# Kernel optimization log

Hardware: AMD Instinct MI355X
Metric: run time of the kernel (lower is better)

The kernel has to match this reference:

```python
import jax, jax.numpy as jnp
import numpy as np

B, N, HW, PS, FHW = 16, 4096, 224, 8, 56

def _gelu(x):
    return jax.nn.gelu(x, approximate=True)  # tanh approximation, matches nn.GELU(approximate='tanh')

def _conv(x, w, b, stride):
    y = jax.lax.conv_general_dilated(x, w, (stride, stride), [(1, 1), (1, 1)],
                                     dimension_numbers=('NCHW', 'OIHW', 'NCHW'))
    return y + b[None, :, None, None]

def _embed(points):
    # for i in 0..11: append sin(2^i * p) then cos(2^i * p) -> [B,N,48]
    factors = 2.0 ** jnp.arange(12, dtype=points.dtype)
    scaled = points[..., None, :] * factors[:, None]          # [B,N,12,2]
    feats = jnp.concatenate([jnp.sin(scaled), jnp.cos(scaled)], axis=-1)  # [B,N,12,4]
    return feats.reshape(points.shape[0], points.shape[1], 48)

def _extract_patches(fmap, points):
    # fmap [B,C,H,W]; points in [0,1]; bilinear grid_sample, zeros padding, align_corners=True
    Bq, C, H, W = fmap.shape
    centers = points * 2.0 - 1.0
    step = 2.0 / (W - 1)
    half = (PS - 1) / 2.0
    offs = jnp.linspace(-half, half, PS, dtype=fmap.dtype) * step
    offx2d, offy2d = jnp.meshgrid(offs, offs, indexing='ij')   # [ps,ps]
    gx = centers[..., 0][..., None, None] + offx2d             # [B,N,ps,ps]
    gy = centers[..., 1][..., None, None] + offy2d
    # align_corners=True pixel coords
    ix = (gx + 1.0) * 0.5 * (W - 1)
    iy = (gy + 1.0) * 0.5 * (H - 1)
    x0f = jnp.floor(ix); y0f = jnp.floor(iy)
    x0 = x0f.astype(jnp.int32); y0 = y0f.astype(jnp.int32)
    x1 = x0 + 1; y1 = y0 + 1
    wx1 = ix - x0f; wx0 = 1.0 - wx1
    wy1 = iy - y0f; wy0 = 1.0 - wy1
    fflat = fmap.reshape(Bq, C, H * W)

    def corner(xi, yi, w):
        valid = ((xi >= 0) & (xi < W) & (yi >= 0) & (yi < H)).astype(fmap.dtype)
        idx = jnp.clip(yi, 0, H - 1) * W + jnp.clip(xi, 0, W - 1)   # [B,N,ps,ps]
        vals = jax.vmap(lambda f, i: f[:, i])(fflat, idx)           # [B,C,N,ps,ps]
        return vals * (w * valid)[:, None]

    out = (corner(x0, y0, wx0 * wy0) + corner(x1, y0, wx1 * wy0)
           + corner(x0, y1, wx0 * wy1) + corner(x1, y1, wx1 * wy1))  # [B,C,N,ps,ps]
    return out.transpose(0, 2, 1, 3, 4)                              # [B,N,C,ps,ps]

def setup_inputs():
    key = jax.random.key(0)
    ks = jax.random.split(key, 26)
    def w(k, shape):
        fan_in = int(np.prod(shape[1:]))
        return jax.random.normal(k, shape, jnp.float32) * (1.0 / np.sqrt(fan_in))
    inp = {
        'points': jax.random.uniform(ks[0], (B, N, 2), jnp.float32),
        'images': jax.random.normal(ks[1], (B, 3, HW, HW), jnp.float32),
        # plane encoder
        'pw1': w(ks[2], (16, 3, 3, 3)),  'pb1': jnp.zeros((16,), jnp.float32),
        'pw2': w(ks[3], (32, 16, 3, 3)), 'pb2': jnp.zeros((32,), jnp.float32),
        'pw3': w(ks[4], (4, 32, 3, 3)),  'pb3': jnp.zeros((4,), jnp.float32),
        # global encoder
        'gw1': w(ks[5], (4, 3, 3, 3)),   'gb1': jnp.zeros((4,), jnp.float32),
        'gw2': w(ks[6], (8, 4, 3, 3)),   'gb2': jnp.zeros((8,), jnp.float32),
        'gw3': w(ks[7], (16, 8, 3, 3)),  'gb3': jnp.zeros((16,), jnp.float32),
        'gw4': w(ks[8], (32, 16, 3, 3)), 'gb4': jnp.zeros((32,), jnp.float32),
        'gw5': w(ks[9], (64, 32, 3, 3)), 'gb5': jnp.zeros((64,), jnp.float32),
        # point encoder (torch Linear: [out,in])
        'lw1': w(ks[10], (256, 48)),  'lb1': jnp.zeros((256,), jnp.float32),
        'lw2': w(ks[11], (256, 256)), 'lb2': jnp.zeros((256,), jnp.float32),
        # head
        'hw1': w(ks[12], (512, 576)), 'hb1': jnp.zeros((512,), jnp.float32),
        'hw2': w(ks[13], (1, 512)),   'hb2': jnp.zeros((1,), jnp.float32),
    }
    return inp

def reference(points, images, pw1, pb1, pw2, pb2, pw3, pb3,
              gw1, gb1, gw2, gb2, gw3, gb3, gw4, gb4, gw5, gb5,
              lw1, lb1, lw2, lb2, hw1, hb1, hw2, hb2):
    # point branch
    pe = _embed(points)                                         # [B,N,48]
    pf = _gelu(pe @ lw1.T + lb1) @ lw2.T + lb2                  # [B,N,256]
    # plane encoder -> 4x56x56 fmap
    f = _gelu(_conv(images, pw1, pb1, 2))
    f = _gelu(_conv(f, pw2, pb2, 2))
    fmap = _gelu(_conv(f, pw3, pb3, 1))                         # [B,4,56,56]
    # global encoder -> [B,64]
    g = images
    for wg, bg in ((gw1, gb1), (gw2, gb2), (gw3, gb3), (gw4, gb4), (gw5, gb5)):
        g = _gelu(_conv(g, wg, bg, 2))
    gc = g.mean(axis=(2, 3))                                    # AvgPool2d(7)+Flatten -> [B,64]
    gc = jnp.broadcast_to(gc[:, None, :], (points.shape[0], points.shape[1], 64))
    # per-point bilinear patch gather
    patches = _extract_patches(fmap, points).reshape(points.shape[0], points.shape[1], -1)  # [B,N,256]
    fused = jnp.concatenate([pf, patches, gc], axis=-1)         # [B,N,576]
    logit = _gelu(fused @ hw1.T + hb1) @ hw2.T + hb2            # [B,N,1]
    return logit
```

## Files before the change

kernel.cpp:

```cpp
#include <hip/hip_runtime.h>
#include <math.h>

#define BB 16
#define NN 4096
#define M_TOT (BB*NN)
#define TBK 32

typedef __attribute__((ext_vector_type(8))) short s8v;
typedef __attribute__((ext_vector_type(4))) float f4v;

__device__ __forceinline__ float gelu_t(float x){
    float u = 1.5957691216057308f * x * (1.0f + 0.044715f*x*x);
    return x / (1.0f + __expf(-u));
}

__device__ __forceinline__ unsigned short f2bf(float f){
    unsigned int u = __float_as_uint(f);
    u += 0x7fffu + ((u >> 16) & 1u);
    return (unsigned short)(u >> 16);
}

#define GLL(src, dst) __builtin_amdgcn_global_load_lds( \
    (const __attribute__((address_space(1))) void*)(src), \
    (__attribute__((address_space(3))) void*)(dst), 16, 0, 0)

template<int CIN, int COUT, int STRIDE, int CHUNK>
__device__ __forceinline__ void conv_dev2(
    const float* __restrict__ in, const float* __restrict__ w,
    const float* __restrict__ bias, float* __restrict__ out,
    int Hin, int Win, int Hout, int Wout, int bx, int by, int b, float* tile)
{
    constexpr int IW = 15*STRIDE + 3;
    constexpr int IH = IW;
    constexpr int PITCH = IW + 1;
    int tid = threadIdx.x;
    int tx = tid & 15, ty = tid >> 4;
    int wo = bx*16 + tx;
    int ho = by*16 + ty;
    int win0 = bx*16*STRIDE - 1;
    int hin0 = by*16*STRIDE - 1;
    bool valid = (wo < Wout) && (ho < Hout);

    float acc[COUT];
    #pragma unroll
    for (int co = 0; co < COUT; ++co) acc[co] = bias[co];

    const float* ib = in + (size_t)(b*CIN)*Hin*Win;
    for (int ci0 = 0; ci0 < CIN; ci0 += CHUNK) {
        __syncthreads();
        for (int idx = tid; idx < CHUNK*IH*IW; idx += 256) {
            int c = idx / (IH*IW), rem = idx - c*(IH*IW);
            int r = rem / IW, cc = rem - r*IW;
            int hi = hin0 + r, wi = win0 + cc;
            float v = 0.f;
            if ((unsigned)hi < (unsigned)Hin && (unsigned)wi < (unsigned)Win)
                v = ib[(size_t)(ci0 + c)*Hin*Win + hi*Win + wi];
            tile[c*IH*PITCH + r*PITCH + cc] = v;
        }
        __syncthreads();
        for (int ci = 0; ci < CHUNK; ++ci) {
            float vv[9];
            const float* tb = tile + ci*IH*PITCH;
            #pragma unroll
            for (int kh = 0; kh < 3; ++kh)
                #pragma unroll
                for (int kw = 0; kw < 3; ++kw)
                    vv[kh*3+kw] = tb[(ty*STRIDE + kh)*PITCH + tx*STRIDE + kw];
            const float* wc = w + (ci0 + ci)*9;
            #pragma unroll
            for (int co = 0; co < COUT; ++co) {
                const float* wp = wc + co*CIN*9;
                #pragma unroll
                for (int k = 0; k < 9; ++k)
                    acc[co] = fmaf(vv[k], wp[k], acc[co]);
            }
        }
    }
    if (valid) {
        size_t obase = ((size_t)b*COUT)*Hout*Wout + (size_t)ho*Wout + wo;
        #pragma unroll
        for (int co = 0; co < COUT; ++co)
            out[obase + (size_t)co*Hout*Wout] = gelu_t(acc[co]);
    }
}

__global__ __launch_bounds__(256) void conv_dual_k(
    const float* __restrict__ in,
    const float* __restrict__ wA, const float* __restrict__ bA,
    const float* __restrict__ wB, const float* __restrict__ bB,
    float* __restrict__ outA, float* __restrict__ outB)
{
    __shared__ float tile[3*33*34];
    const int Hin = 224, Win = 224, Hout = 112, Wout = 112;
    int tid = threadIdx.x;
    int tx = tid & 15, ty = tid >> 4;
    int b = blockIdx.z;
    int wo = blockIdx.x*16 + tx;
    int ho = blockIdx.y*16 + ty;
    int win0 = blockIdx.x*32 - 1;
    int hin0 = blockIdx.y*32 - 1;

    const float* ib = in + (size_t)(b*3)*Hin*Win;
    for (int idx = tid; idx < 3*1089; idx += 256) {
        int c = idx / 1089, rem = idx - c*1089;
        int r = rem / 33, cc = rem - r*33;
        int hi = hin0 + r, wi = win0 + cc;
        float v = 0.f;
        if ((unsigned)hi < (unsigned)Hin && (unsigned)wi < (unsigned)Win)
            v = ib[(size_t)c*Hin*Win + hi*Win + wi];
        tile[c*33*34 + r*34 + cc] = v;
    }
    __syncthreads();

    float accA[16], accB[4];
    #pragma unroll
    for (int co = 0; co < 16; ++co) accA[co] = bA[co];
    #pragma unroll
    for (int co = 0; co < 4; ++co) accB[co] = bB[co];

    #pragma unroll
    for (int ci = 0; ci < 3; ++ci) {
        float vv[9];
        const float* tb = tile + ci*33*34;
        #pragma unroll
        for (int kh = 0; kh < 3; ++kh)
            #pragma unroll
            for (int kw = 0; kw < 3; ++kw)
                vv[kh*3+kw] = tb[(ty*2 + kh)*34 + tx*2 + kw];
        #pragma unroll
        for (int co = 0; co < 16; ++co) {
            const float* wp = wA + co*27 + ci*9;
            #pragma unroll
            for (int k = 0; k < 9; ++k) accA[co] = fmaf(vv[k], wp[k], accA[co]);
        }
        #pragma unroll
        for (int co = 0; co < 4; ++co) {
            const float* wp = wB + co*27 + ci*9;
            #pragma unroll
            for (int k = 0; k < 9; ++k) accB[co] = fmaf(vv[k], wp[k], accB[co]);
        }
    }
    size_t px = (size_t)ho*Wout + wo;
    #pragma unroll
    for (int co = 0; co < 16; ++co)
        outA[((size_t)(b*16 + co))*Hout*Wout + px] = gelu_t(accA[co]);
    #pragma unroll
    for (int co = 0; co < 4; ++co)
        outB[((size_t)(b*4 + co))*Hout*Wout + px] = gelu_t(accB[co]);
}

__global__ __launch_bounds__(256) void conv_pg2_k(
    const float* __restrict__ f1, const float* __restrict__ pw2, const float* __restrict__ pb2, float* __restrict__ f2,
    const float* __restrict__ g1, const float* __restrict__ gw2, const float* __restrict__ gb2, float* __restrict__ g2)
{
    __shared__ float tile[8*33*34];
    int z = blockIdx.z;
    if (z < 32) {
        int b = z >> 1, half = z & 1;
        conv_dev2<16,16,2,8>(f1 + (size_t)b*16*12544, pw2 + half*2304, pb2 + half*16,
                             f2 + ((size_t)(b*32 + half*16))*3136,
                             112,112, 56,56, blockIdx.x, blockIdx.y, 0, tile);
    } else {
        conv_dev2<4,8,2,4>(g1, gw2, gb2, g2, 112,112, 56,56, blockIdx.x, blockIdx.y, z-32, tile);
    }
}

__global__ __launch_bounds__(256) void conv_pg3_k(
    const float* __restrict__ f2, const float* __restrict__ pw3, const float* __restrict__ pb3, float4* __restrict__ fmap4,
    const float* __restrict__ g2, const float* __restrict__ gw3, const float* __restrict__ gb3, float* __restrict__ g3)
{
    __shared__ float tile[8*33*34];
    int z = blockIdx.z;
    if (z < 16) {
        int b = z;
        int idx = blockIdx.x*256 + threadIdx.x;
        if (idx >= 3136) return;
        int ho = idx / 56, wo = idx - ho*56;
        const float* ib = f2 + (size_t)b*32*3136;
        float acc[4];
        #pragma unroll
        for (int co = 0; co < 4; ++co) acc[co] = pb3[co];
        for (int ci = 0; ci < 32; ++ci) {
            const float* ic = ib + (size_t)ci*3136;
            #pragma unroll
            for (int kh = 0; kh < 3; ++kh) {
                int hi = ho - 1 + kh;
                if ((unsigned)hi >= 56u) continue;
                #pragma unroll
                for (int kw = 0; kw < 3; ++kw) {
                    int wi = wo - 1 + kw;
                    if ((unsigned)wi >= 56u) continue;
                    float v = ic[hi*56 + wi];
                    int wofs = ci*9 + kh*3 + kw;
                    #pragma unroll
                    for (int co = 0; co < 4; ++co)
                        acc[co] = fmaf(v, pw3[co*288 + wofs], acc[co]);
                }
            }
        }
        float4 o;
        o.x = gelu_t(acc[0]); o.y = gelu_t(acc[1]);
        o.z = gelu_t(acc[2]); o.w = gelu_t(acc[3]);
        fmap4[(size_t)b*3136 + idx] = o;
    } else {
        if (blockIdx.x >= 4) return;
        int bx = blockIdx.x & 1, by = blockIdx.x >> 1;
        conv_dev2<8,16,2,8>(g2, gw3, gb3, g3, 56,56, 28,28, bx, by, z-16, tile);
    }
}

__global__ __launch_bounds__(256) void g4_k(
    const float* __restrict__ g3, const float* __restrict__ w4,
    const float* __restrict__ b4, float* __restrict__ g4o)
{
    int idx = blockIdx.x*256 + threadIdx.x;
    int co = idx & 31;
    int t = idx >> 5;
    int b = t / 196, px = t - b*196;
    int ho = px / 14, wo = px - ho*14;
    const float* src = g3 + (size_t)b*16*784;
    const float* wp = w4 + co*144;
    float acc = b4[co];
    for (int ci = 0; ci < 16; ++ci) {
        #pragma unroll
        for (int kh = 0; kh < 3; ++kh) {
            int hi = ho*2 - 1 + kh;
            if ((unsigned)hi >= 28u) continue;
            #pragma unroll
            for (int kw = 0; kw < 3; ++kw) {
                int wi = wo*2 - 1 + kw;
                if ((unsigned)wi >= 28u) continue;
                acc = fmaf(src[ci*784 + hi*28 + wi], wp[ci*9 + kh*3 + kw], acc);
            }
        }
    }
    g4o[(size_t)b*6272 + px*32 + co] = gelu_t(acc);
}

__global__ __launch_bounds__(256) void g5_k(
    const float* __restrict__ g4o, const float* __restrict__ w5,
    const float* __restrict__ b5, float* __restrict__ gc)
{
    int idx = blockIdx.x*256 + threadIdx.x;
    int co = idx & 63;
    int t = idx >> 6;
    int b = t / 49, px = t - b*49;
    int ho = px / 7, wo = px - ho*7;
    const float* src = g4o + (size_t)b*6272;
    const float* wp = w5 + co*288;
    float acc = b5[co];
    for (int ci = 0; ci < 32; ++ci) {
        #pragma unroll
        for (int kh = 0; kh < 3; ++kh) {
            int hi = ho*2 - 1 + kh;
            if ((unsigned)hi >= 14u) continue;
            #pragma unroll
            for (int kw = 0; kw < 3; ++kw) {
                int wi = wo*2 - 1 + kw;
                if ((unsigned)wi >= 14u) continue;
                acc = fmaf(src[(hi*14 + wi)*32 + ci], wp[ci*9 + kh*3 + kw], acc);
            }
        }
    }
    atomicAdd(&gc[b*64 + co], gelu_t(acc) * (1.0f/49.0f));
}

__global__ void cvtall_k(const float* __restrict__ lw1, const float* __restrict__ lw2,
                         const float* __restrict__ hw1, unsigned short* __restrict__ blw1,
                         unsigned short* __restrict__ blw2, unsigned short* __restrict__ bhw1,
                         float* __restrict__ out, const float* __restrict__ b2,
                         float* __restrict__ gc){
    int i = blockIdx.x*blockDim.x + threadIdx.x;
    if (i < M_TOT) out[i] = b2[0];
    if (i < 1024) gc[i] = 0.f;
    if (i < 256*64) {
        int r = i >> 6, c = i & 63;
        blw1[i] = (c < 48) ? f2bf(lw1[r*48 + c]) : 0;
        return;
    }
    int j = i - 256*64;
    if (j < 256*256) { blw2[j] = f2bf(lw2[j]); return; }
    j -= 256*256;
    if (j < 512*576) bhw1[j] = f2bf(hw1[j]);
}

__global__ __launch_bounds__(512) void mlp12_k(
    const float* __restrict__ points,
    const unsigned short* __restrict__ W1, const float* __restrict__ b1,
    const unsigned short* __restrict__ W2, const float* __restrict__ b2,
    unsigned short* __restrict__ C,
    const float4* __restrict__ fmap4, const float* __restrict__ gc)
{
    __shared__ unsigned short Hd[128*256];
    __shared__ unsigned short B2[256*TBK];
    int tid = threadIdx.x;
    int wv = tid >> 6, lane = tid & 63;
    int q = lane >> 4, lr = lane & 15;
    int mi = wv >> 2, ni = wv & 3;
    size_t m0 = (size_t)blockIdx.x * 128;

    f4v acc1[4][4];
    #pragma unroll
    for (int i = 0; i < 4; ++i)
        #pragma unroll
        for (int j = 0; j < 4; ++j) acc1[i][j] = (f4v){0.f,0.f,0.f,0.f};

    #pragma unroll
    for (int kb = 0; kb < 2; ++kb) {
        int seg = kb*4 + q;
        s8v a[4], b[4];
        #pragma unroll
        for (int t = 0; t < 4; ++t) {
            size_t m = m0 + mi*64 + t*16 + lr;
            float px = points[m*2], py = points[m*2+1];
            union { s8v v; unsigned short u[8]; } pk;
            #pragma unroll
            for (int j = 0; j < 8; ++j) {
                int k = seg*8 + j;
                unsigned short val = 0;
                if (k < 48) {
                    int i2 = k >> 2, rr = k & 3;
                    float f = (float)(1 << i2);
                    float p = (rr & 1) ? py : px;
                    float s = f * p;
                    val = f2bf((rr < 2) ? __sinf(s) : __cosf(s));
                }
                pk.u[j] = val;
            }
            a[t] = pk.v;
        }
        #pragma unroll
        for (int t = 0; t < 4; ++t) {
            int n = ni*64 + t*16 + lr;
            b[t] = *(const s8v*)(W1 + n*64 + seg*8);
        }
        #pragma unroll
        for (int mt = 0; mt < 4; ++mt)
            #pragma unroll
            for (int nt = 0; nt < 4; ++nt)
                acc1[mt][nt] = __builtin_amdgcn_mfma_f32_16x16x32_bf16(a[mt], b[nt], acc1[mt][nt], 0, 0, 0);
    }
    {
        float b1v[4];
        #pragma unroll
        for (int nt = 0; nt < 4; ++nt) b1v[nt] = b1[ni*64 + nt*16 + lr];
        #pragma unroll
        for (int mt = 0; mt < 4; ++mt)
            #pragma unroll
            for (int r4 = 0; r4 < 4; ++r4) {
                int row = mi*64 + mt*16 + q*4 + r4;
                #pragma unroll
                for (int nt = 0; nt < 4; ++nt) {
                    int col = ni*64 + nt*16 + lr;
                    float v = gelu_t(acc1[mt][nt][r4] + b1v[nt]);
                    int p = (col >> 3) ^ (row & 7);
                    Hd[(row*32 + p)*8 + (col & 7)] = f2bf(v);
                }
            }
    }
    __syncthreads();

    f4v acc2[4][4];
    #pragma unroll
    for (int i = 0; i < 4; ++i)
        #pragma unroll
        for (int j = 0; j < 4; ++j) acc2[i][j] = (f4v){0.f,0.f,0.f,0.f};

    for (int kt = 0; kt < 8; ++kt) {
        #pragma unroll
        for (int r = 0; r < 2; ++r) {
            int f = r*512 + tid;
            int rr = f >> 2, ll = (f & 3) ^ ((f >> 3) & 3);
            GLL(W2 + rr*256 + kt*32 + ll*8, B2 + f*8);
        }
        __syncthreads();
        s8v a[4], b[4];
        int sw = q ^ ((lr >> 1) & 3);
        #pragma unroll
        for (int t = 0; t < 4; ++t) {
            int row = mi*64 + t*16 + lr;
            int p = (kt*4 + q) ^ (row & 7);
            a[t] = *(const s8v*)(Hd + (row*32 + p)*8);
        }
        #pragma unroll
        for (int t = 0; t < 4; ++t) {
            int n = ni*64 + t*16 + lr;
            b[t] = *(const s8v*)(B2 + (n*4 + sw)*8);
        }
        #pragma unroll
        for (int mt = 0; mt < 4; ++mt)
            #pragma unroll
            for (int nt = 0; nt < 4; ++nt)
                acc2[mt][nt] = __builtin_amdgcn_mfma_f32_16x16x32_bf16(a[mt], b[nt], acc2[mt][nt], 0, 0, 0);
        __syncthreads();
    }
    {
        float b2v[4];
        #pragma unroll
        for (int nt = 0; nt < 4; ++nt) b2v[nt] = b2[ni*64 + nt*16 + lr];
        #pragma unroll
        for (int mt = 0; mt < 4; ++mt)
            #pragma unroll
            for (int r4 = 0; r4 < 4; ++r4) {
                size_t m = m0 + mi*64 + mt*16 + q*4 + r4;
                #pragma unroll
                for (int nt = 0; nt < 4; ++nt) {
                    int n = ni*64 + nt*16 + lr;
                    C[m*576 + n] = f2bf(acc2[mt][nt][r4] + b2v[nt]);
                }
            }
    }
    #pragma unroll 1
    for (int it = 0; it < 16; ++it) {
        int task = it*512 + tid;
        int ml = task >> 6, ij = task & 63;
        size_t m = m0 + ml;
        int i = ij >> 3, j = ij & 7;
        int b = (int)(m >> 12);
        float px = points[m*2], py = points[m*2+1];
        float cx = px*2.f - 1.f, cy = py*2.f - 1.f;
        const float step = 2.0f/55.0f;
        float gx = cx + ((float)i - 3.5f)*step;
        float gy = cy + ((float)j - 3.5f)*step;
        float ix = (gx + 1.f)*0.5f*55.f;
        float iy = (gy + 1.f)*0.5f*55.f;
        float x0f = floorf(ix), y0f = floorf(iy);
        int x0 = (int)x0f, y0 = (int)y0f;
        int x1 = x0 + 1,  y1 = y0 + 1;
        float wx1 = ix - x0f, wx0 = 1.f - wx1;
        float wy1 = iy - y0f, wy0 = 1.f - wy1;
        float v00 = ((x0>=0)&&(x0<56)&&(y0>=0)&&(y0<56)) ? 1.f : 0.f;
        float v10 = ((x1>=0)&&(x1<56)&&(y0>=0)&&(y0<56)) ? 1.f : 0.f;
        float v01 = ((x0>=0)&&(x0<56)&&(y1>=0)&&(y1<56)) ? 1.f : 0.f;
        float v11 = ((x1>=0)&&(x1<56)&&(y1>=0)&&(y1<56)) ? 1.f : 0.f;
        float w00 = wx0*wy0*v00, w10 = wx1*wy0*v10, w01 = wx0*wy1*v01, w11 = wx1*wy1*v11;
        int cx0 = min(max(x0,0),55), cx1 = min(max(x1,0),55);
        int cy0 = min(max(y0,0),55), cy1 = min(max(y1,0),55);
        const float4* fb = fmap4 + (size_t)b*3136;
        float4 f00 = fb[cy0*56 + cx0], f10 = fb[cy0*56 + cx1];
        float4 f01 = fb[cy1*56 + cx0], f11 = fb[cy1*56 + cx1];
        float4 v;
        v.x = w00*f00.x + w10*f10.x + w01*f01.x + w11*f11.x;
        v.y = w00*f00.y + w10*f10.y + w01*f01.y + w11*f11.y;
        v.z = w00*f00.z + w10*f10.z + w01*f01.z + w11*f11.z;
        v.w = w00*f00.w + w10*f10.w + w01*f01.w + w11*f11.w;
        C[m*576 + 256 +   0 + ij] = f2bf(v.x);
        C[m*576 + 256 +  64 + ij] = f2bf(v.y);
        C[m*576 + 256 + 128 + ij] = f2bf(v.z);
        C[m*576 + 256 + 192 + ij] = f2bf(v.w);
        C[m*576 + 512 + ij] = f2bf(gc[b*64 + ij]);
    }
}

__global__ __launch_bounds__(256, 3) void gemm_hd_k(
    const unsigned short* __restrict__ A,
    const unsigned short* __restrict__ W,
    const float* __restrict__ bias, const float* __restrict__ w2,
    float* __restrict__ out)
{
    __shared__ unsigned short As[64*TBK];
    __shared__ unsigned short Bs[256*TBK];
    __shared__ float red[4*64];
    int tid = threadIdx.x;
    int wv = tid >> 6, lane = tid & 63;
    int q = lane >> 4, lr = lane & 15;
    int sw = q ^ ((lr >> 1) & 3);
    int nq = wv * 64;
    size_t m0 = (size_t)blockIdx.x * 64;
    int nbase = blockIdx.y * 256;

    int rA = tid >> 2;
    int lA = (tid & 3) ^ ((tid >> 3) & 3);
    const unsigned short* srcA = A + (m0 + rA)*576 + lA*8;
    unsigned short* dstA = As + tid*8;
    const unsigned short* srcB[4]; unsigned short* dstB[4];
    #pragma unroll
    for (int r = 0; r < 4; ++r) {
        int f = r*256 + tid;
        int rr = f >> 2, ll = (f & 3) ^ ((f >> 3) & 3);
        srcB[r] = W + (size_t)(nbase + rr)*576 + ll*8;
        dstB[r] = Bs + f*8;
    }

    f4v acc[4][4];
    #pragma unroll
    for (int i = 0; i < 4; ++i)
        #pragma unroll
        for (int j = 0; j < 4; ++j) acc[i][j] = (f4v){0.f,0.f,0.f,0.f};

    for (int k0 = 0; k0 < 576; k0 += TBK) {
        GLL(srcA, dstA); srcA += TBK;
        #pragma unroll
        for (int r = 0; r < 4; ++r) { GLL(srcB[r], dstB[r]); srcB[r] += TBK; }
        __syncthreads();
        s8v a[4], b[4];
        #pragma unroll
        for (int t = 0; t < 4; ++t)
            a[t] = *(const s8v*)(As + (t*16 + lr)*TBK + sw*8);
        #pragma unroll
        for (int t = 0; t < 4; ++t)
            b[t] = *(const s8v*)(Bs + (nq + t*16 + lr)*TBK + sw*8);
        #pragma unroll
        for (int mt = 0; mt < 4; ++mt)
            #pragma unroll
            for (int nt = 0; nt < 4; ++nt)
                acc[mt][nt] = __builtin_amdgcn_mfma_f32_16x16x32_bf16(a[mt], b[nt], acc[mt][nt], 0, 0, 0);
        __syncthreads();
    }
    float bv[4], w2v[4];
    #pragma unroll
    for (int nt = 0; nt < 4; ++nt) {
        int n = nbase + nq + nt*16 + lr;
        bv[nt] = bias[n];
        w2v[nt] = w2[n];
    }
    #pragma unroll
    for (int mt = 0; mt < 4; ++mt)
        #pragma unroll
        for (int r4 = 0; r4 < 4; ++r4) {
            int ml = mt*16 + q*4 + r4;
            float s = 0.f;
            #pragma unroll
            for (int nt = 0; nt < 4; ++nt)
                s += gelu_t(acc[mt][nt][r4] + bv[nt]) * w2v[nt];
            #pragma unroll
            for (int off = 8; off > 0; off >>= 1) s += __shfl_down(s, off, 16);
            if (lr == 0) red[wv*64 + ml] = s;
        }
    __syncthreads();
    if (tid < 64) {
        float t = red[tid] + red[64 + tid] + red[128 + tid] + red[192 + tid];
        atomicAdd(&out[m0 + tid], t);
    }
}

extern "C" void kernel_launch(void* const* d_in, const int* in_sizes, int n_in,
                              void* d_out, int out_size, void* d_ws, size_t ws_size,
                              hipStream_t stream) {
    const float* points = (const float*)d_in[0];
    const float* images = (const float*)d_in[1];
    const float* pw1 = (const float*)d_in[2];  const float* pb1 = (const float*)d_in[3];
    const float* pw2 = (const float*)d_in[4];  const float* pb2 = (const float*)d_in[5];
    const float* pw3 = (const float*)d_in[6];  const float* pb3 = (const float*)d_in[7];
    const float* gw1 = (const float*)d_in[8];  const float* gb1 = (const float*)d_in[9];
    const float* gw2 = (const float*)d_in[10]; const float* gb2 = (const float*)d_in[11];
    const float* gw3 = (const float*)d_in[12]; const float* gb3 = (const float*)d_in[13];
    const float* gw4 = (const float*)d_in[14]; const float* gb4 = (const float*)d_in[15];
    const float* gw5 = (const float*)d_in[16]; const float* gb5 = (const float*)d_in[17];
    const float* lw1 = (const float*)d_in[18]; const float* lb1 = (const float*)d_in[19];
    const float* lw2 = (const float*)d_in[20]; const float* lb2 = (const float*)d_in[21];
    const float* hw1 = (const float*)d_in[22]; const float* hb1 = (const float*)d_in[23];
    const float* hw2 = (const float*)d_in[24]; const float* hb2 = (const float*)d_in[25];
    float* out = (float*)d_out;

    char* base = (char*)d_ws;
    unsigned short* fused_b = (unsigned short*)base;
    unsigned short* hid_b   = fused_b + (size_t)M_TOT*576;
    float4* fmap4 = (float4*)(hid_b + (size_t)M_TOT*256);
    float* gc   = (float*)(fmap4 + (size_t)16*3136);
    unsigned short* blw1 = (unsigned short*)(gc + 1024);
    unsigned short* blw2 = blw1 + 256*64;
    unsigned short* bhw1 = blw2 + 256*256;
    float* ct = (float*)base;
    float* f1 = ct;
    float* f2 = f1 + (size_t)16*16*112*112;
    float* g1 = f2 + (size_t)16*32*56*56;
    float* g2 = g1 + (size_t)16*4*112*112;
    float* g3 = g2 + (size_t)16*8*56*56;
    float* g4 = g3 + (size_t)16*16*28*28;

    cvtall_k<<<1472, 256, 0, stream>>>(lw1, lw2, hw1, blw1, blw2, bhw1, out, hb2, gc);
    conv_dual_k<<<dim3(7,7,16), 256, 0, stream>>>(images, pw1, pb1, gw1, gb1, f1, g1);
    conv_pg2_k<<<dim3(4,4,48), 256, 0, stream>>>(f1, pw2, pb2, f2, g1, gw2, gb2, g2);
    conv_pg3_k<<<dim3(13,1,32), 256, 0, stream>>>(f2, pw3, pb3, fmap4, g2, gw3, gb3, g3);
    g4_k<<<392, 256, 0, stream>>>(g3, gw4, gb4, g4);
    g5_k<<<196, 256, 0, stream>>>(g4, gw5, gb5, gc);
    mlp12_k<<<M_TOT/128, 512, 0, stream>>>(points, blw1, lb1, blw2, lb2, fused_b, fmap4, gc);
    gemm_hd_k<<<dim3(M_TOT/64, 2), 256, 0, stream>>>(fused_b, bhw1, hb1, hw2, out);
}
```

Baseline: 433.3 us.

## Fuse point MLP, patch gather and head GEMM into one kernel via LDS

Merges mlp12_k and gemm_hd_k into a single mega kernel. Each 64-row tile now keeps its 576-wide fused feature row in swizzled LDS instead of writing it to a global bf16 buffer and reading it back. Each block covers all 512 head outputs, so the final sum is written directly with the bias instead of atomically added, and the output init is dropped from cvtall_k. The cost is a large LDS footprint (about 105 KB) that limits occupancy, more accumulators per wave (4x8 tiles), and W2 B-fragments read straight from global memory without LDS staging.

Result: slower. 486.1 us (+12.2%).

```diff
diff --git a/kernel.cpp b/kernel.cpp
--- a/kernel.cpp
+++ b/kernel.cpp
@@ -23,6 +23,12 @@
 #define GLL(src, dst) __builtin_amdgcn_global_load_lds( \
     (const __attribute__((address_space(1))) void*)(src), \
     (__attribute__((address_space(3))) void*)(dst), 16, 0, 0)
+
+__device__ __forceinline__ int fs_addr(int row, int col){
+    int chunk = col >> 3;
+    int ph = (chunk & ~7) | ((chunk & 7) ^ (row & 7));
+    return row*576 + ph*8 + (col & 7);
+}
 
 template<int CIN, int COUT, int STRIDE, int CHUNK>
 __device__ __forceinline__ void conv_dev2(
@@ -268,10 +274,8 @@
 __global__ void cvtall_k(const float* __restrict__ lw1, const float* __restrict__ lw2,
                          const float* __restrict__ hw1, unsigned short* __restrict__ blw1,
                          unsigned short* __restrict__ blw2, unsigned short* __restrict__ bhw1,
-                         float* __restrict__ out, const float* __restrict__ b2,
                          float* __restrict__ gc){
     int i = blockIdx.x*blockDim.x + threadIdx.x;
-    if (i < M_TOT) out[i] = b2[0];
     if (i < 1024) gc[i] = 0.f;
     if (i < 256*64) {
         int r = i >> 6, c = i & 63;
@@ -284,135 +288,128 @@
     if (j < 512*576) bhw1[j] = f2bf(hw1[j]);
 }
 
-__global__ __launch_bounds__(512) void mlp12_k(
+__global__ __launch_bounds__(256) void mega_k(
     const float* __restrict__ points,
     const unsigned short* __restrict__ W1, const float* __restrict__ b1,
     const unsigned short* __restrict__ W2, const float* __restrict__ b2,
-    unsigned short* __restrict__ C,
-    const float4* __restrict__ fmap4, const float* __restrict__ gc)
-{
-    __shared__ unsigned short Hd[128*256];
-    __shared__ unsigned short B2[256*TBK];
+    const unsigned short* __restrict__ WH, const float* __restrict__ bh,
+    const float* __restrict__ w2h, const float* __restrict__ b2h,
+    const float4* __restrict__ fmap4, const float* __restrict__ gc,
+    float* __restrict__ out)
+{
+    __shared__ unsigned short Fs[64*576];
+    __shared__ unsigned short Sc[64*256];
+    __shared__ float red[4*64];
     int tid = threadIdx.x;
     int wv = tid >> 6, lane = tid & 63;
     int q = lane >> 4, lr = lane & 15;
-    int mi = wv >> 2, ni = wv & 3;
-    size_t m0 = (size_t)blockIdx.x * 128;
-
-    f4v acc1[4][4];
-    #pragma unroll
-    for (int i = 0; i < 4; ++i)
-        #pragma unroll
-        for (int j = 0; j < 4; ++j) acc1[i][j] = (f4v){0.f,0.f,0.f,0.f};
-
-    #pragma unroll
-    for (int kb = 0; kb < 2; ++kb) {
-        int seg = kb*4 + q;
-        s8v a[4], b[4];
-        #pragma unroll
-        for (int t = 0; t < 4; ++t) {
-            size_t m = m0 + mi*64 + t*16 + lr;
-            float px = points[m*2], py = points[m*2+1];
-            union { s8v v; unsigned short u[8]; } pk;
-            #pragma unroll
-            for (int j = 0; j < 8; ++j) {
-                int k = seg*8 + j;
-                unsigned short val = 0;
-                if (k < 48) {
-                    int i2 = k >> 2, rr = k & 3;
-                    float f = (float)(1 << i2);
-                    float p = (rr & 1) ? py : px;
-                    float s = f * p;
-                    val = f2bf((rr < 2) ? __sinf(s) : __cosf(s));
+    int nq = wv * 64;
+    size_t m0 = (size_t)blockIdx.x * 64;
+
+    {
+        f4v acc1[4][4];
+        #pragma unroll
+        for (int i = 0; i < 4; ++i)
+            #pragma unroll
+            for (int j = 0; j < 4; ++j) acc1[i][j] = (f4v){0.f,0.f,0.f,0.f};
+        #pragma unroll
+        for (int kb = 0; kb < 2; ++kb) {
+            int seg = kb*4 + q;
+            s8v a[4], b[4];
+            #pragma unroll
+            for (int t = 0; t < 4; ++t) {
+                size_t m = m0 + t*16 + lr;
+                float px = points[m*2], py = points[m*2+1];
+                union { s8v v; unsigned short u[8]; } pk;
+                #pragma unroll
+                for (int j = 0; j < 8; ++j) {
+                    int k = seg*8 + j;
+                    unsigned short val = 0;
+                    if (k < 48) {
+                        int i2 = k >> 2, rr = k & 3;
+                        float f = (float)(1 << i2);
+                        float p = (rr & 1) ? py : px;
+                        float s = f * p;
+                        val = f2bf((rr < 2) ? __sinf(s) : __cosf(s));
+                    }
+                    pk.u[j] = val;
                 }
-                pk.u[j] = val;
-            }
-            a[t] = pk.v;
-        }
-        #pragma unroll
-        for (int t = 0; t < 4; ++t) {
-            int n = ni*64 + t*16 + lr;
-            b[t] = *(const s8v*)(W1 + n*64 + seg*8);
-        }
+                a[t] = pk.v;
+            }
+            #pragma unroll
+            for (int t = 0; t < 4; ++t) {
+                int n = nq + t*16 + lr;
+                b[t] = *(const s8v*)(W1 + n*64 + seg*8);
+            }
+            #pragma unroll
+            for (int mt = 0; mt < 4; ++mt)
+                #pragma unroll
+                for (int nt = 0; nt < 4; ++nt)
+                    acc1[mt][nt] = __builtin_amdgcn_mfma_f32_16x16x32_bf16(a[mt], b[nt], acc1[mt][nt], 0, 0, 0);
+        }
+        float b1v[4];
+        #pragma unroll
+        for (int nt = 0; nt < 4; ++nt) b1v[nt] = b1[nq + nt*16 + lr];
         #pragma unroll
         for (int mt = 0; mt < 4; ++mt)
             #pragma unroll
-            for (int nt = 0; nt < 4; ++nt)
-                acc1[mt][nt] = __builtin_amdgcn_mfma_f32_16x16x32_bf16(a[mt], b[nt], acc1[mt][nt], 0, 0, 0);
-    }
-    {
-        float b1v[4];
-        #pragma unroll
-        for (int nt = 0; nt < 4; ++nt) b1v[nt] = b1[ni*64 + nt*16 + lr];
-        #pragma unroll
-        for (int mt = 0; mt < 4; ++mt)
-            #pragma unroll
             for (int r4 = 0; r4 < 4; ++r4) {
-                int row = mi*64 + mt*16 + q*4 + r4;
+                int row = mt*16 + q*4 + r4;
                 #pragma unroll
                 for (int nt = 0; nt < 4; ++nt) {
-                    int col = ni*64 + nt*16 + lr;
+                    int col = nq + nt*16 + lr;
                     float v = gelu_t(acc1[mt][nt][r4] + b1v[nt]);
                     int p = (col >> 3) ^ (row & 7);
-                    Hd[(row*32 + p)*8 + (col & 7)] = f2bf(v);
+                    Sc[(row*32 + p)*8 + (col & 7)] = f2bf(v);
                 }
             }
     }
     __syncthreads();
 
-    f4v acc2[4][4];
-    #pragma unroll
-    for (int i = 0; i < 4; ++i)
-        #pragma unroll
-        for (int j = 0; j < 4; ++j) acc2[i][j] = (f4v){0.f,0.f,0.f,0.f};
-
-    for (int kt = 0; kt < 8; ++kt) {
-        #pragma unroll
-        for (int r = 0; r < 2; ++r) {
-            int f = r*512 + tid;
-            int rr = f >> 2, ll = (f & 3) ^ ((f >> 3) & 3);
-            GLL(W2 + rr*256 + kt*32 + ll*8, B2 + f*8);
-        }
-        __syncthreads();
-        s8v a[4], b[4];
-        int sw = q ^ ((lr >> 1) & 3);
-        #pragma unroll
-        for (int t = 0; t < 4; ++t) {
-            int row = mi*64 + t*16 + lr;
-            int p = (kt*4 + q) ^ (row & 7);
-            a[t] = *(const s8v*)(Hd + (row*32 + p)*8);
-        }
-        #pragma unroll
-        for (int t = 0; t < 4; ++t) {
-            int n = ni*64 + t*16 + lr;
-            b[t] = *(const s8v*)(B2 + (n*4 + sw)*8);
-        }
+    {
+        f4v acc2[4][4];
+        #pragma unroll
+        for (int i = 0; i < 4; ++i)
+            #pragma unroll
+            for (int j = 0; j < 4; ++j) acc2[i][j] = (f4v){0.f,0.f,0.f,0.f};
+        for (int kt = 0; kt < 8; ++kt) {
+            s8v a[4], b[4];
+            #pragma unroll
+            for (int t = 0; t < 4; ++t) {
+                int row = t*16 + lr;
+                int p = (kt*4 + q) ^ (row & 7);
+                a[t] = *(const s8v*)(Sc + (row*32 + p)*8);
+            }
+            #pragma unroll
+            for (int t = 0; t < 4; ++t) {
+                int n = nq + t*16 + lr;
+                b[t] = *(const s8v*)(W2 + (size_t)n*256 + kt*32 + q*8);
+            }
+            #pragma unroll
+            for (int mt = 0; mt < 4; ++mt)
+                #pragma unroll
+                for (int nt = 0; nt < 4; ++nt)
+                    acc2[mt][nt] = __builtin_amdgcn_mfma_f32_16x16x32_bf16(a[mt], b[nt], acc2[mt][nt], 0, 0, 0);
+        }
+        float b2v[4];
+        #pragma unroll
+        for (int nt = 0; nt < 4; ++nt) b2v[nt] = b2[nq + nt*16 + lr];
         #pragma unroll
         for (int mt = 0; mt < 4; ++mt)
             #pragma unroll
-            for (int nt = 0; nt < 4; ++nt)
-                acc2[mt][nt] = __builtin_amdgcn_mfma_f32_16x16x32_bf16(a[mt], b[nt], acc2[mt][nt], 0, 0, 0);
-        __syncthreads();
-    }
-    {
-        float b2v[4];
-        #pragma unroll
-        for (int nt = 0; nt < 4; ++nt) b2v[nt] = b2[ni*64 + nt*16 + lr];
-        #pragma unroll
-        for (int mt = 0; mt < 4; ++mt)
-            #pragma unroll
             for (int r4 = 0; r4 < 4; ++r4) {
-                size_t m = m0 + mi*64 + mt*16 + q*4 + r4;
+                int row = mt*16 + q*4 + r4;
                 #pragma unroll
                 for (int nt = 0; nt < 4; ++nt) {
-                    int n = ni*64 + nt*16 + lr;
-                    C[m*576 + n] = f2bf(acc2[mt][nt][r4] + b2v[nt]);
+                    int col = nq + nt*16 + lr;
+                    Fs[fs_addr(row, col)] = f2bf(acc2[mt][nt][r4] + b2v[nt]);
                 }
             }
     }
+
     #pragma unroll 1
     for (int it = 0; it < 16; ++it) {
-        int task = it*512 + tid;
+        int task = it*256 + tid;
         int ml = task >> 6, ij = task & 63;
         size_t m = m0 + ml;
         int i = ij >> 3, j = ij & 7;
@@ -444,93 +441,82 @@
         v.y = w00*f00.y + w10*f10.y + w01*f01.y + w11*f11.y;
         v.z = w00*f00.z + w10*f10.z + w01*f01.z + w11*f11.z;
         v.w = w00*f00.w + w10*f10.w + w01*f01.w + w11*f11.w;
-        C[m*576 + 256 +   0 + ij] = f2bf(v.x);
-        C[m*576 + 256 +  64 + ij] = f2bf(v.y);
-        C[m*576 + 256 + 128 + ij] = f2bf(v.z);
-        C[m*576 + 256 + 192 + ij] = f2bf(v.w);
-        C[m*576 + 512 + ij] = f2bf(gc[b*64 + ij]);
-    }
-}
-
-__global__ __launch_bounds__(256, 3) void gemm_hd_k(
-    const unsigned short* __restrict__ A,
-    const unsigned short* __restrict__ W,
-    const float* __restrict__ bias, const float* __restrict__ w2,
-    float* __restrict__ out)
-{
-    __shared__ unsigned short As[64*TBK];
-    __shared__ unsigned short Bs[256*TBK];
-    __shared__ float red[4*64];
-    int tid = threadIdx.x;
-    int wv = tid >> 6, lane = tid & 63;
-    int q = lane >> 4, lr = lane & 15;
-    int sw = q ^ ((lr >> 1) & 3);
-    int nq = wv * 64;
-    size_t m0 = (size_t)blockIdx.x * 64;
-    int nbase = blockIdx.y * 256;
-
-    int rA = tid >> 2;
-    int lA = (tid & 3) ^ ((tid >> 3) & 3);
-    const unsigned short* srcA = A + (m0 + rA)*576 + lA*8;
-    unsigned short* dstA = As + tid*8;
-    const unsigned short* srcB[4]; unsigned short* dstB[4];
-    #pragma unroll
-    for (int r = 0; r < 4; ++r) {
-        int f = r*256 + tid;
-        int rr = f >> 2, ll = (f & 3) ^ ((f >> 3) & 3);
-        srcB[r] = W + (size_t)(nbase + rr)*576 + ll*8;
-        dstB[r] = Bs + f*8;
-    }
-
-    f4v acc[4][4];
-    #pragma unroll
-    for (int i = 0; i < 4; ++i)
-        #pragma unroll
-        for (int j = 0; j < 4; ++j) acc[i][j] = (f4v){0.f,0.f,0.f,0.f};
-
-    for (int k0 = 0; k0 < 576; k0 += TBK) {
-        GLL(srcA, dstA); srcA += TBK;
-        #pragma unroll
-        for (int r = 0; r < 4; ++r) { GLL(srcB[r], dstB[r]); srcB[r] += TBK; }
+        Fs[fs_addr(ml, 256 +   0 + ij)] = f2bf(v.x);
+        Fs[fs_addr(ml, 256 +  64 + ij)] = f2bf(v.y);
+        Fs[fs_addr(ml, 256 + 128 + ij)] = f2bf(v.z);
+        Fs[fs_addr(ml, 256 + 192 + ij)] = f2bf(v.w);
+        Fs[fs_addr(ml, 512 + ij)] = f2bf(gc[b*64 + ij]);
+    }
+    __syncthreads();
+
+    {
+        int nq2 = wv * 128;
+        int sw = q ^ ((lr >> 1) & 3);
+        f4v acc[4][8];
+        #pragma unroll
+        for (int i = 0; i < 4; ++i)
+            #pragma unroll
+            for (int j = 0; j < 8; ++j) acc[i][j] = (f4v){0.f,0.f,0.f,0.f};
+
+        const unsigned short* srcB[8]; unsigned short* dstB[8];
+        #pragma unroll
+        for (int r = 0; r < 8; ++r) {
+            int f = r*256 + tid;
+            int rr = f >> 2, ll = (f & 3) ^ ((f >> 3) & 3);
+            srcB[r] = WH + (size_t)rr*576 + ll*8;
+            dstB[r] = Sc + f*8;
+        }
+
+        for (int k0 = 0; k0 < 576; k0 += TBK) {
+            #pragma unroll
+            for (int r = 0; r < 8; ++r) { GLL(srcB[r], dstB[r]); srcB[r] += TBK; }
+            __syncthreads();
+            s8v a[4], b[8];
+            int cbase = k0 >> 3;
+            #pragma unroll
+            for (int t = 0; t < 4; ++t) {
+                int row = t*16 + lr;
+                int chunk = cbase + q;
+                int ph = (chunk & ~7) | ((chunk & 7) ^ (row & 7));
+                a[t] = *(const s8v*)(Fs + row*576 + ph*8);
+            }
+            #pragma unroll
+            for (int t = 0; t < 8; ++t) {
+                int n = nq2 + t*16 + lr;
+                b[t] = *(const s8v*)(Sc + (n*4 + sw)*8);
+            }
+            #pragma unroll
+            for (int mt = 0; mt < 4; ++mt)
+                #pragma unroll
+                for (int nt = 0; nt < 8; ++nt)
+                    acc[mt][nt] = __builtin_amdgcn_mfma_f32_16x16x32_bf16(a[mt], b[nt], acc[mt][nt], 0, 0, 0);
+            __syncthreads();
+        }
+        float bv[8], w2v[8];
+        #pragma unroll
+        for (int nt = 0; nt < 8; ++nt) {
+            int n = nq2 + nt*16 + lr;
+            bv[nt] = bh[n];
+            w2v[nt] = w2h[n];
+        }
+        #pragma unroll
+        for (int mt = 0; mt < 4; ++mt)
+            #pragma unroll
+            for (int r4 = 0; r4 < 4; ++r4) {
+                int ml = mt*16 + q*4 + r4;
+                float s = 0.f;
+                #pragma unroll
+                for (int nt = 0; nt < 8; ++nt)
+                    s += gelu_t(acc[mt][nt][r4] + bv[nt]) * w2v[nt];
+                #pragma unroll
+                for (int off = 8; off > 0; off >>= 1) s += __shfl_down(s, off, 16);
+                if (lr == 0) red[wv*64 + ml] = s;
+            }
         __syncthreads();
-        s8v a[4], b[4];
-        #pragma unroll
-        for (int t = 0; t < 4; ++t)
-            a[t] = *(const s8v*)(As + (t*16 + lr)*TBK + sw*8);
-        #pragma unroll
-        for (int t = 0; t < 4; ++t)
-            b[t] = *(const s8v*)(Bs + (nq + t*16 + lr)*TBK + sw*8);
-        #pragma unroll
-        for (int mt = 0; mt < 4; ++mt)
-            #pragma unroll
-            for (int nt = 0; nt < 4; ++nt)
-                acc[mt][nt] = __builtin_amdgcn_mfma_f32_16x16x32_bf16(a[mt], b[nt], acc[mt][nt], 0, 0, 0);
-        __syncthreads();
-    }
-    float bv[4], w2v[4];
-    #pragma unroll
-    for (int nt = 0; nt < 4; ++nt) {
-        int n = nbase + nq + nt*16 + lr;
-        bv[nt] = bias[n];
-        w2v[nt] = w2[n];
-    }
-    #pragma unroll
-    for (int mt = 0; mt < 4; ++mt)
-        #pragma unroll
-        for (int r4 = 0; r4 < 4; ++r4) {
-            int ml = mt*16 + q*4 + r4;
-            float s = 0.f;
-            #pragma unroll
-            for (int nt = 0; nt < 4; ++nt)
-                s += gelu_t(acc[mt][nt][r4] + bv[nt]) * w2v[nt];
-            #pragma unroll
-            for (int off = 8; off > 0; off >>= 1) s += __shfl_down(s, off, 16);
-            if (lr == 0) red[wv*64 + ml] = s;
-        }
-    __syncthreads();
-    if (tid < 64) {
-        float t = red[tid] + red[64 + tid] + red[128 + tid] + red[192 + tid];
-        atomicAdd(&out[m0 + tid], t);
+        if (tid < 64) {
+            float t = red[tid] + red[64 + tid] + red[128 + tid] + red[192 + tid];
+            out[m0 + tid] = t + b2h[0];
+        }
     }
 }
 
@@ -554,8 +540,8 @@
     float* out = (float*)d_out;
 
     char* base = (char*)d_ws;
-    unsigned short* fused_b = (unsigned short*)base;
-    unsigned short* hid_b   = fused_b + (size_t)M_TOT*576;
+    unsigned short* spacer = (unsigned short*)base;
+    unsigned short* hid_b  = spacer + (size_t)M_TOT*576;
     float4* fmap4 = (float4*)(hid_b + (size_t)M_TOT*256);
     float* gc   = (float*)(fmap4 + (size_t)16*3136);
     unsigned short* blw1 = (unsigned short*)(gc + 1024);
@@ -569,12 +555,12 @@
     float* g3 = g2 + (size_t)16*8*56*56;
     float* g4 = g3 + (size_t)16*16*28*28;
 
-    cvtall_k<<<1472, 256, 0, stream>>>(lw1, lw2, hw1, blw1, blw2, bhw1, out, hb2, gc);
+    cvtall_k<<<1472, 256, 0, stream>>>(lw1, lw2, hw1, blw1, blw2, bhw1, gc);
     conv_dual_k<<<dim3(7,7,16), 256, 0, stream>>>(images, pw1, pb1, gw1, gb1, f1, g1);
     conv_pg2_k<<<dim3(4,4,48), 256, 0, stream>>>(f1, pw2, pb2, f2, g1, gw2, gb2, g2);
     conv_pg3_k<<<dim3(13,1,32), 256, 0, stream>>>(f2, pw3, pb3, fmap4, g2, gw3, gb3, g3);
     g4_k<<<392, 256, 0, stream>>>(g3, gw4, gb4, g4);
     g5_k<<<196, 256, 0, stream>>>(g4, gw5, gb5, gc);
-    mlp12_k<<<M_TOT/128, 512, 0, stream>>>(points, blw1, lb1, blw2, lb2, fused_b, fmap4, gc);
-    gemm_hd_k<<<dim3(M_TOT/64, 2), 256, 0, stream>>>(fused_b, bhw1, hb1, hw2, out);
-}
+    mega_k<<<M_TOT/64, 256, 0, stream>>>(points, blw1, lb1, blw2, lb2,
+                                         bhw1, hb1, hw2, hb2, fmap4, gc, out);
+}
```
